# Kernel tuning notes

Hardware: AMD Instinct MI355X
Metric: run time of the kernel (lower is better)

The kernel has to match this reference:

```python
import jax, jax.numpy as jnp
import numpy as np

B, S, D = 2, 1024, 1024
E = 8          # routed experts
I = 1024       # per-expert intermediate
IS = 1024      # shared expert intermediate
TOP_K = 2
NUM_SHARED = 1


def setup_inputs() -> dict:
    key = jax.random.key(0)
    ks = jax.random.split(key, 8)
    scale = 0.02
    return {
        "x": jax.random.normal(ks[0], (B, S, D), dtype=jnp.float32),
        "w_gate": jax.random.normal(ks[1], (D, E), dtype=jnp.float32) * scale,
        "wg": jax.random.normal(ks[2], (E, D, I), dtype=jnp.float32) * scale,  # expert gate_proj
        "wu": jax.random.normal(ks[3], (E, D, I), dtype=jnp.float32) * scale,  # expert up_proj
        "wd": jax.random.normal(ks[4], (E, I, D), dtype=jnp.float32) * scale,  # expert down_proj
        "ws_g": jax.random.normal(ks[5], (NUM_SHARED, D, IS), dtype=jnp.float32) * scale,
        "ws_u": jax.random.normal(ks[6], (NUM_SHARED, D, IS), dtype=jnp.float32) * scale,
        "ws_d": jax.random.normal(ks[7], (NUM_SHARED, IS, D), dtype=jnp.float32) * scale,
    }


def _swiglu(t, w_gate_proj, w_up, w_down):
    # t: [N, D]
    g = t @ w_gate_proj            # [N, I]
    u = t @ w_up                   # [N, I]
    return (jax.nn.silu(g) * u) @ w_down  # [N, D]


def reference(x, w_gate, wg, wu, wd, ws_g, ws_u, ws_d):
    Bb, Ss, Dd = x.shape
    x_flat = x.reshape(Bb * Ss, Dd)                  # [N, D]
    N = x_flat.shape[0]

    # --- router ---
    logits = x_flat @ w_gate                          # [N, E]
    topk_logits, topk_idx = jax.lax.top_k(logits, TOP_K)
    topk_w = jax.nn.softmax(topk_logits, axis=-1)     # [N, K]

    # --- aux load-balancing loss ---
    one_hot = jax.nn.one_hot(topk_idx, E, dtype=jnp.float32)  # [N, K, E]
    f = one_hot.sum(axis=1).mean(axis=0)                       # [E]
    P = jax.nn.softmax(logits, axis=-1).mean(axis=0)           # [E]
    aux_loss = E * jnp.sum(f * P)

    # --- combine weights: cw[n, e] = sum_k topk_w[n,k] * 1[topk_idx[n,k]==e] ---
    cw = jnp.einsum("nk,nke->ne", topk_w, one_hot)             # [N, E]

    # --- routed experts: dense compute over all experts, weighted combine ---
    g = jnp.einsum("nd,edi->eni", x_flat, wg)                  # [E, N, I]
    u = jnp.einsum("nd,edi->eni", x_flat, wu)                  # [E, N, I]
    a = jax.nn.silu(g) * u                                     # [E, N, I]
    y = jnp.einsum("eni,eid->end", a, wd)                      # [E, N, D]
    routed = jnp.einsum("ne,end->nd", cw, y)                   # [N, D]

    # --- shared experts ---
    shared = jnp.zeros_like(x_flat)
    for s in range(NUM_SHARED):
        shared = shared + _swiglu(x_flat, ws_g[s], ws_u[s], ws_d[s])

    out = (routed + shared).reshape(Bb, Ss, Dd)
    return out, aux_loss
```

## Files before the change

### kernel.cpp

```cpp
#include <hip/hip_runtime.h>
#include <math.h>

typedef unsigned short u16;
typedef __attribute__((ext_vector_type(8))) short short8;
typedef __attribute__((ext_vector_type(4))) float f32x4;
typedef __attribute__((ext_vector_type(4))) unsigned short u16x4;
typedef __attribute__((ext_vector_type(8))) unsigned short u16x8;

#define N_TOK 2048
#define DIM 1024
#define OUT_ELEMS 2097152

#define GLDS16(gp, lp) __builtin_amdgcn_global_load_lds( \
    (const __attribute__((address_space(1))) unsigned int*)(gp), \
    (__attribute__((address_space(3))) unsigned int*)(lp), 16, 0, 0)

__device__ __forceinline__ u16 f2bf(float f) {
    union { float f; unsigned u; } v; v.f = f;
    unsigned r = (v.u + 0x7FFFu + ((v.u >> 16) & 1u)) >> 16;
    return (u16)r;
}
__device__ __forceinline__ float bf2f(u16 h) {
    union { unsigned u; float f; } v; v.u = ((unsigned)h) << 16;
    return v.f;
}

__global__ void k_cvt_x(const float* __restrict__ x, u16* __restrict__ xb,
                        int* __restrict__ tlist, int* __restrict__ curs,
                        float* __restrict__ Psum, int* __restrict__ cnt8) {
    int i = blockIdx.x * 256 + threadIdx.x;
    f32x4 v = ((const f32x4*)x)[i];
    u16x4 o;
    o.x = f2bf(v.x); o.y = f2bf(v.y); o.z = f2bf(v.z); o.w = f2bf(v.w);
    ((u16x4*)xb)[i] = o;
    if (i < 2048) tlist[4096 + i] = i;
    if (i < 16) curs[i] = 0;
    if (i < 8) { Psum[i] = 0.f; cnt8[i] = 0; }
}

__global__ void k_cvt_w(const float* __restrict__ wg, const float* __restrict__ wu,
                        const float* __restrict__ wd, const float* __restrict__ wsg,
                        const float* __restrict__ wsu, const float* __restrict__ wsd,
                        u16* __restrict__ wgt, u16* __restrict__ wut,
                        u16* __restrict__ wdt, u16* __restrict__ wsgt,
                        u16* __restrict__ wsut, u16* __restrict__ wsdt) {
    __shared__ float tile[64 * 65];
    int bx = blockIdx.x;
    int mat = bx >> 8;
    int tl  = bx & 255;
    int tr = tl >> 4, tc = tl & 15;
    const float* src; u16* dst;
    if      (mat <  8) { src = wg  + (size_t)mat * 1048576;        dst = wgt + (size_t)mat * 1048576; }
    else if (mat < 16) { src = wu  + (size_t)(mat - 8) * 1048576;  dst = wut + (size_t)(mat - 8) * 1048576; }
    else if (mat < 24) { src = wd  + (size_t)(mat - 16) * 1048576; dst = wdt + (size_t)(mat - 16) * 1048576; }
    else if (mat == 24){ src = wsg; dst = wsgt; }
    else if (mat == 25){ src = wsu; dst = wsut; }
    else               { src = wsd; dst = wsdt; }
    int t = threadIdx.x;
    int col = (t & 15) * 4;
    int r0  = t >> 4;
#pragma unroll
    for (int j = 0; j < 4; j++) {
        int row = r0 + j * 16;
        f32x4 v = *(const f32x4*)(src + (size_t)(tr * 64 + row) * 1024 + tc * 64 + col);
        float* tp = tile + row * 65 + col;
        tp[0] = v.x; tp[1] = v.y; tp[2] = v.z; tp[3] = v.w;
    }
    __syncthreads();
    int kc = (t & 7) * 8;
#pragma unroll
    for (int it = 0; it < 2; it++) {
        int orow = (t >> 3) + it * 32;
        u16x8 o;
#pragma unroll
        for (int i = 0; i < 8; i++) o[i] = f2bf(tile[(kc + i) * 65 + orow]);
        *(u16x8*)(dst + (size_t)(tc * 64 + orow) * 1024 + tr * 64 + kc) = o;
    }
}

__global__ void k_router(const float* __restrict__ x, const float* __restrict__ wgate,
                         int* __restrict__ tidx, float* __restrict__ tw,
                         float* __restrict__ Psum, int* __restrict__ cnt8) {
    __shared__ float sP[8];
    __shared__ int   sC[8];
    int t = threadIdx.x;
    if (t < 8) { sP[t] = 0.f; sC[t] = 0; }
    __syncthreads();
    int wave = t >> 6;
    int lane = t & 63;
    int n = blockIdx.x * 4 + wave;
    const float* xr = x + (size_t)n * DIM;
    float acc[8] = {0.f,0.f,0.f,0.f,0.f,0.f,0.f,0.f};
    for (int d = lane; d < DIM; d += 64) {
        float xv = xr[d];
        const float* wr = wgate + d * 8;
#pragma unroll
        for (int e = 0; e < 8; e++) acc[e] += xv * wr[e];
    }
#pragma unroll
    for (int off = 32; off; off >>= 1) {
#pragma unroll
        for (int e = 0; e < 8; e++) acc[e] += __shfl_xor(acc[e], off);
    }
    if (lane == 0) {
        float mx = acc[0];
#pragma unroll
        for (int e = 1; e < 8; e++) mx = fmaxf(mx, acc[e]);
        float p[8], s = 0.f;
#pragma unroll
        for (int e = 0; e < 8; e++) { p[e] = expf(acc[e] - mx); s += p[e]; }
        float inv = 1.f / s;
#pragma unroll
        for (int e = 0; e < 8; e++) atomicAdd(&sP[e], p[e] * inv);
        int i0 = 0; float b0 = acc[0];
#pragma unroll
        for (int e = 1; e < 8; e++) if (acc[e] > b0) { b0 = acc[e]; i0 = e; }
        int i1 = -1; float b1 = -3.4e38f;
#pragma unroll
        for (int e = 0; e < 8; e++) if (e != i0 && acc[e] > b1) { b1 = acc[e]; i1 = e; }
        float w0 = 1.f / (1.f + expf(b1 - b0));
        tidx[n * 2] = i0; tidx[n * 2 + 1] = i1;
        tw[n * 2] = w0;   tw[n * 2 + 1] = 1.f - w0;
        atomicAdd(&sC[i0], 1);
        atomicAdd(&sC[i1], 1);
    }
    __syncthreads();
    if (t < 8) {
        atomicAdd(&Psum[t], sP[t]);
        atomicAdd(&cnt8[t], sC[t]);
    }
}

__global__ void k_scatter(const int* __restrict__ tidx, const float* __restrict__ Psum,
                          const int* __restrict__ cnt8, int* __restrict__ curs,
                          int* __restrict__ tlist, int* __restrict__ slots,
                          float* __restrict__ out, int* __restrict__ counts,
                          int* __restrict__ offs) {
    __shared__ int s_off[8];
    int t = threadIdx.x;
    if (t == 0) {
        int o = 0;
        for (int e = 0; e < 8; e++) { s_off[e] = o; o += cnt8[e]; }
    }
    __syncthreads();
    if (blockIdx.x == 0 && t == 0) {
        float aux = 0.f;
        for (int e = 0; e < 8; e++) {
            int c = cnt8[e];
            aux += (float)c * Psum[e];
            offs[e] = s_off[e]; counts[e] = c;
        }
        out[OUT_ELEMS] = 8.f * aux / ((float)N_TOK * (float)N_TOK);
        offs[8] = 4096; counts[8] = 2048;
    }
    int n = blockIdx.x * 256 + t;
    if (n < N_TOK) {
#pragma unroll
        for (int k = 0; k < 2; k++) {
            int e = tidx[n * 2 + k];
            int p = atomicAdd(&curs[e], 1);
            int sl = s_off[e] + p;
            tlist[sl] = n;
            slots[n * 2 + k] = sl;
        }
    }
}

__global__ __launch_bounds__(256, 2)
void k_gemm1(const u16* __restrict__ xb, const u16* __restrict__ wgt,
             const u16* __restrict__ wut, const u16* __restrict__ wsgt,
             const u16* __restrict__ wsut, const int* __restrict__ tlist,
             const int* __restrict__ counts, const int* __restrict__ offs,
             u16* __restrict__ H) {
    int bx = blockIdx.x;
    int job = bx >> 7;
    int mt = (bx >> 3) & 15;
    int nt = bx & 7;
    int jcnt = counts[job];
    int m0 = mt << 7;
    if (m0 >= jcnt) return;
    int joff = offs[job];
    int n0 = nt << 7;
    const u16* Bg = (job < 8) ? (wgt + (size_t)job * 1048576) : wsgt;
    const u16* Bu = (job < 8) ? (wut + (size_t)job * 1048576) : wsut;

    __shared__ __attribute__((aligned(128))) u16 As[4096];
    __shared__ __attribute__((aligned(128))) u16 Bgs[4096];
    __shared__ __attribute__((aligned(128))) u16 Bus[4096];

    int t = threadIdx.x;
    int wave = t >> 6, lane = t & 63;
    int ch = (lane & 3) * 8;
    int r0 = (wave * 2 + 0) * 16 + (lane >> 2);
    int r1 = (wave * 2 + 1) * 16 + (lane >> 2);
    int tok0 = tlist[joff + m0 + r0];
    int tok1 = tlist[joff + m0 + r1];
    const u16* a0 = xb + (size_t)tok0 * 1024 + ch;
    const u16* a1 = xb + (size_t)tok1 * 1024 + ch;
    const u16* g0 = Bg + (size_t)(n0 + r0) * 1024 + ch;
    const u16* g1 = Bg + (size_t)(n0 + r1) * 1024 + ch;
    const u16* u0 = Bu + (size_t)(n0 + r0) * 1024 + ch;
    const u16* u1 = Bu + (size_t)(n0 + r1) * 1024 + ch;
    u16* lA0 = As  + (wave * 2 + 0) * 512;  u16* lA1 = As  + (wave * 2 + 1) * 512;
    u16* lG0 = Bgs + (wave * 2 + 0) * 512;  u16* lG1 = Bgs + (wave * 2 + 1) * 512;
    u16* lU0 = Bus + (wave * 2 + 0) * 512;  u16* lU1 = Bus + (wave * 2 + 1) * 512;

    int wm = (wave >> 1) << 6, wn = (wave & 1) << 6;
    int quad = lane >> 4, lr = lane & 15;

    f32x4 accg[4][4], accu[4][4];
    f32x4 zz = {0.f, 0.f, 0.f, 0.f};
#pragma unroll
    for (int i = 0; i < 4; i++)
#pragma unroll
        for (int j = 0; j < 4; j++) { accg[i][j] = zz; accu[i][j] = zz; }

    for (int k0 = 0; k0 < 1024; k0 += 32) {
        GLDS16(a0 + k0, lA0);  GLDS16(a1 + k0, lA1);
        GLDS16(g0 + k0, lG0);  GLDS16(g1 + k0, lG1);
        GLDS16(u0 + k0, lU0);  GLDS16(u1 + k0, lU1);
        __syncthreads();
        short8 af[4], bgf[4], buf[4];
#pragma unroll
        for (int i = 0; i < 4; i++) {
            af[i]  = *(const short8*)(As  + (wm + i * 16 + lr) * 32 + quad * 8);
            bgf[i] = *(const short8*)(Bgs + (wn + i * 16 + lr) * 32 + quad * 8);
            buf[i] = *(const short8*)(Bus + (wn + i * 16 + lr) * 32 + quad * 8);
        }
#pragma unroll
        for (int mi = 0; mi < 4; mi++)
#pragma unroll
            for (int ni = 0; ni < 4; ni++) {
                accg[mi][ni] = __builtin_amdgcn_mfma_f32_16x16x32_bf16(af[mi], bgf[ni], accg[mi][ni], 0, 0, 0);
                accu[mi][ni] = __builtin_amdgcn_mfma_f32_16x16x32_bf16(af[mi], buf[ni], accu[mi][ni], 0, 0, 0);
            }
        __syncthreads();
    }
#pragma unroll
    for (int mi = 0; mi < 4; mi++) {
        int rowb = m0 + wm + mi * 16 + quad * 4;
#pragma unroll
        for (int rr = 0; rr < 4; rr++) {
            int row = rowb + rr;
            if (row < jcnt) {
                size_t base = (size_t)(joff + row) * 1024 + n0 + wn;
#pragma unroll
                for (int ni = 0; ni < 4; ni++) {
                    float g = accg[mi][ni][rr];
                    float u = accu[mi][ni][rr];
                    float h = (g / (1.f + expf(-g))) * u;
                    H[base + ni * 16 + lr] = f2bf(h);
                }
            }
        }
    }
}

__global__ __launch_bounds__(256, 2)
void k_gemm2(const u16* __restrict__ H, const u16* __restrict__ wdt,
             const u16* __restrict__ wsdt, const int* __restrict__ counts,
             const int* __restrict__ offs, u16* __restrict__ Y) {
    int bx = blockIdx.x;
    int job = bx >> 7;
    int mt = (bx >> 3) & 15;
    int nt = bx & 7;
    int jcnt = counts[job];
    int m0 = mt << 7;
    if (m0 >= jcnt) return;
    int joff = offs[job];
    int n0 = nt << 7;
    const u16* Bt = (job < 8) ? (wdt + (size_t)job * 1048576) : wsdt;

    __shared__ __attribute__((aligned(128))) u16 As[4096];
    __shared__ __attribute__((aligned(128))) u16 Bs[4096];

    int t = threadIdx.x;
    int wave = t >> 6, lane = t & 63;
    int ch = (lane & 3) * 8;
    int r0 = (wave * 2 + 0) * 16 + (lane >> 2);
    int r1 = (wave * 2 + 1) * 16 + (lane >> 2);
    const u16* a0 = H + (size_t)(joff + m0 + r0) * 1024 + ch;
    const u16* a1 = H + (size_t)(joff + m0 + r1) * 1024 + ch;
    const u16* b0 = Bt + (size_t)(n0 + r0) * 1024 + ch;
    const u16* b1 = Bt + (size_t)(n0 + r1) * 1024 + ch;
    u16* lA0 = As + (wave * 2 + 0) * 512;  u16* lA1 = As + (wave * 2 + 1) * 512;
    u16* lB0 = Bs + (wave * 2 + 0) * 512;  u16* lB1 = Bs + (wave * 2 + 1) * 512;

    int wm = (wave >> 1) << 6, wn = (wave & 1) << 6;
    int quad = lane >> 4, lr = lane & 15;

    f32x4 acc[4][4];
    f32x4 zz = {0.f, 0.f, 0.f, 0.f};
#pragma unroll
    for (int i = 0; i < 4; i++)
#pragma unroll
        for (int j = 0; j < 4; j++) acc[i][j] = zz;

    for (int k0 = 0; k0 < 1024; k0 += 32) {
        GLDS16(a0 + k0, lA0);  GLDS16(a1 + k0, lA1);
        GLDS16(b0 + k0, lB0);  GLDS16(b1 + k0, lB1);
        __syncthreads();
        short8 af[4], bf[4];
#pragma unroll
        for (int i = 0; i < 4; i++) {
            af[i] = *(const short8*)(As + (wm + i * 16 + lr) * 32 + quad * 8);
            bf[i] = *(const short8*)(Bs + (wn + i * 16 + lr) * 32 + quad * 8);
        }
#pragma unroll
        for (int mi = 0; mi < 4; mi++)
#pragma unroll
            for (int ni = 0; ni < 4; ni++)
                acc[mi][ni] = __builtin_amdgcn_mfma_f32_16x16x32_bf16(af[mi], bf[ni], acc[mi][ni], 0, 0, 0);
        __syncthreads();
    }
#pragma unroll
    for (int mi = 0; mi < 4; mi++) {
        int rowb = m0 + wm + mi * 16 + quad * 4;
#pragma unroll
        for (int rr = 0; rr < 4; rr++) {
            int row = rowb + rr;
            if (row < jcnt) {
                u16* yrow = Y + (size_t)(joff + row) * 1024 + n0 + wn;
#pragma unroll
                for (int ni = 0; ni < 4; ni++)
                    yrow[ni * 16 + lr] = f2bf(acc[mi][ni][rr]);
            }
        }
    }
}

__global__ void k_combine(const u16* __restrict__ Y, const int* __restrict__ slots,
                          const float* __restrict__ tw, float* __restrict__ out) {
    int n = blockIdx.x;
    int d = threadIdx.x;
    int s0 = slots[n * 2], s1 = slots[n * 2 + 1];
    float w0 = tw[n * 2], w1 = tw[n * 2 + 1];
    u16x4 y0 = ((const u16x4*)(Y + (size_t)s0 * 1024))[d];
    u16x4 y1 = ((const u16x4*)(Y + (size_t)s1 * 1024))[d];
    u16x4 ys = ((const u16x4*)(Y + (size_t)(4096 + n) * 1024))[d];
    f32x4 r;
    r.x = w0 * bf2f(y0.x) + w1 * bf2f(y1.x) + bf2f(ys.x);
    r.y = w0 * bf2f(y0.y) + w1 * bf2f(y1.y) + bf2f(ys.y);
    r.z = w0 * bf2f(y0.z) + w1 * bf2f(y1.z) + bf2f(ys.z);
    r.w = w0 * bf2f(y0.w) + w1 * bf2f(y1.w) + bf2f(ys.w);
    ((f32x4*)(out + (size_t)n * 1024))[d] = r;
}

extern "C" void kernel_launch(void* const* d_in, const int* in_sizes, int n_in,
                              void* d_out, int out_size, void* d_ws, size_t ws_size,
                              hipStream_t stream) {
    const float* x     = (const float*)d_in[0];
    const float* wgate = (const float*)d_in[1];
    const float* wg    = (const float*)d_in[2];
    const float* wu    = (const float*)d_in[3];
    const float* wd    = (const float*)d_in[4];
    const float* wsg   = (const float*)d_in[5];
    const float* wsu   = (const float*)d_in[6];
    const float* wsd   = (const float*)d_in[7];
    float* out = (float*)d_out;

    char* ws = (char*)d_ws;
    u16*   xb    = (u16*)(ws + 0);
    u16*   wgt   = (u16*)(ws + 4194304);
    u16*   wut   = (u16*)(ws + 20971520);
    u16*   wdt   = (u16*)(ws + 37748736);
    u16*   wsgt  = (u16*)(ws + 54525952);
    u16*   wsut  = (u16*)(ws + 56623104);
    u16*   wsdt  = (u16*)(ws + 58720256);
    u16*   H     = (u16*)(ws + 60817408);
    u16*   Y     = (u16*)(ws + 4194304);
    int*   tidx  = (int*)(ws + 73400320);
    float* tw    = (float*)(ws + 73416704);
    int*   tlist = (int*)(ws + 73433088);
    int*   slots = (int*)(ws + 73457664);
    int*   counts= (int*)(ws + 73474048);
    int*   offs  = (int*)(ws + 73474112);
    int*   curs  = (int*)(ws + 73474176);
    float* Psum  = (float*)(ws + 73474240);
    int*   cnt8  = (int*)(ws + 73474304);

    k_cvt_x<<<2048, 256, 0, stream>>>(x, xb, tlist, curs, Psum, cnt8);
    k_router<<<512, 256, 0, stream>>>(x, wgate, tidx, tw, Psum, cnt8);
    k_scatter<<<8, 256, 0, stream>>>(tidx, Psum, cnt8, curs, tlist, slots,
                                     out, counts, offs);
    k_cvt_w<<<6912, 256, 0, stream>>>(wg, wu, wd, wsg, wsu, wsd,
                                      wgt, wut, wdt, wsgt, wsut, wsdt);
    k_gemm1<<<1152, 256, 0, stream>>>(xb, wgt, wut, wsgt, wsut, tlist, counts, offs, H);
    k_gemm2<<<1152, 256, 0, stream>>>(H, wdt, wsdt, counts, offs, Y);
    k_combine<<<2048, 256, 0, stream>>>(Y, slots, tw, out);
}
```

Measured before the change: 280.2 us.

## Fuse x bf16 conversion into router and enlarge weight transpose tiles

Removes the standalone x conversion kernel by writing bf16 x inside the router, which already reads x, leaving a tiny init kernel. Rewrites the weight transpose-convert kernel to use 128x128 tiles, converting to bf16 before storing in shared memory and issuing 16 independent loads per thread. This targets the bandwidth-bound weight conversion and launch overhead, at the cost of more registers and shared memory per block and possible LDS bank conflicts on 16-bit column reads.

```diff
diff --git a/kernel.cpp b/kernel.cpp
--- a/kernel.cpp
+++ b/kernel.cpp
@@ -25,15 +25,10 @@
     return v.f;
 }
 
-__global__ void k_cvt_x(const float* __restrict__ x, u16* __restrict__ xb,
-                        int* __restrict__ tlist, int* __restrict__ curs,
-                        float* __restrict__ Psum, int* __restrict__ cnt8) {
+__global__ void k_init(int* __restrict__ tlist, int* __restrict__ curs,
+                       float* __restrict__ Psum, int* __restrict__ cnt8) {
     int i = blockIdx.x * 256 + threadIdx.x;
-    f32x4 v = ((const f32x4*)x)[i];
-    u16x4 o;
-    o.x = f2bf(v.x); o.y = f2bf(v.y); o.z = f2bf(v.z); o.w = f2bf(v.w);
-    ((u16x4*)xb)[i] = o;
-    if (i < 2048) tlist[4096 + i] = i;
+    tlist[4096 + i] = i;
     if (i < 16) curs[i] = 0;
     if (i < 8) { Psum[i] = 0.f; cnt8[i] = 0; }
 }
@@ -44,11 +39,11 @@
                         u16* __restrict__ wgt, u16* __restrict__ wut,
                         u16* __restrict__ wdt, u16* __restrict__ wsgt,
                         u16* __restrict__ wsut, u16* __restrict__ wsdt) {
-    __shared__ float tile[64 * 65];
+    __shared__ u16 tile[128 * 136];
     int bx = blockIdx.x;
-    int mat = bx >> 8;
-    int tl  = bx & 255;
-    int tr = tl >> 4, tc = tl & 15;
+    int mat = bx >> 6;
+    int tl  = bx & 63;
+    int tr = tl >> 3, tc = tl & 7;
     const float* src; u16* dst;
     if      (mat <  8) { src = wg  + (size_t)mat * 1048576;        dst = wgt + (size_t)mat * 1048576; }
     else if (mat < 16) { src = wu  + (size_t)(mat - 8) * 1048576;  dst = wut + (size_t)(mat - 8) * 1048576; }
@@ -57,30 +52,39 @@
     else if (mat == 25){ src = wsu; dst = wsut; }
     else               { src = wsd; dst = wsdt; }
     int t = threadIdx.x;
-    int col = (t & 15) * 4;
-    int r0  = t >> 4;
-#pragma unroll
-    for (int j = 0; j < 4; j++) {
-        int row = r0 + j * 16;
-        f32x4 v = *(const f32x4*)(src + (size_t)(tr * 64 + row) * 1024 + tc * 64 + col);
-        float* tp = tile + row * 65 + col;
-        tp[0] = v.x; tp[1] = v.y; tp[2] = v.z; tp[3] = v.w;
+    int col = (t & 31) * 4;
+    int rb  = t >> 5;
+    const float* sp = src + (size_t)(tr * 128) * 1024 + tc * 128 + col;
+
+    f32x4 v[16];
+#pragma unroll
+    for (int j = 0; j < 16; j++)
+        v[j] = *(const f32x4*)(sp + (size_t)(j * 8 + rb) * 1024);
+#pragma unroll
+    for (int j = 0; j < 16; j++) {
+        int row = j * 8 + rb;
+        u16x4 o;
+        o.x = f2bf(v[j].x); o.y = f2bf(v[j].y); o.z = f2bf(v[j].z); o.w = f2bf(v[j].w);
+        *(u16x4*)(tile + row * 136 + col) = o;
     }
     __syncthreads();
-    int kc = (t & 7) * 8;
-#pragma unroll
-    for (int it = 0; it < 2; it++) {
-        int orow = (t >> 3) + it * 32;
+    int n  = t & 127;
+    int kb = (t >> 7) * 64;
+    u16* drow = dst + (size_t)(tc * 128 + n) * 1024 + tr * 128;
+#pragma unroll
+    for (int j = 0; j < 8; j++) {
+        int kc = kb + j * 8;
         u16x8 o;
 #pragma unroll
-        for (int i = 0; i < 8; i++) o[i] = f2bf(tile[(kc + i) * 65 + orow]);
-        *(u16x8*)(dst + (size_t)(tc * 64 + orow) * 1024 + tr * 64 + kc) = o;
+        for (int i = 0; i < 8; i++) o[i] = tile[(kc + i) * 136 + n];
+        *(u16x8*)(drow + kc) = o;
     }
 }
 
 __global__ void k_router(const float* __restrict__ x, const float* __restrict__ wgate,
-                         int* __restrict__ tidx, float* __restrict__ tw,
-                         float* __restrict__ Psum, int* __restrict__ cnt8) {
+                         u16* __restrict__ xb, int* __restrict__ tidx,
+                         float* __restrict__ tw, float* __restrict__ Psum,
+                         int* __restrict__ cnt8) {
     __shared__ float sP[8];
     __shared__ int   sC[8];
     int t = threadIdx.x;
@@ -90,9 +94,13 @@
     int lane = t & 63;
     int n = blockIdx.x * 4 + wave;
     const float* xr = x + (size_t)n * DIM;
+    u16* xbr = xb + (size_t)n * DIM;
     float acc[8] = {0.f,0.f,0.f,0.f,0.f,0.f,0.f,0.f};
-    for (int d = lane; d < DIM; d += 64) {
+#pragma unroll
+    for (int i = 0; i < 16; i++) {
+        int d = lane + i * 64;
         float xv = xr[d];
+        xbr[d] = f2bf(xv);
         const float* wr = wgate + d * 8;
 #pragma unroll
         for (int e = 0; e < 8; e++) acc[e] += xv * wr[e];
@@ -379,11 +387,11 @@
     float* Psum  = (float*)(ws + 73474240);
     int*   cnt8  = (int*)(ws + 73474304);
 
-    k_cvt_x<<<2048, 256, 0, stream>>>(x, xb, tlist, curs, Psum, cnt8);
-    k_router<<<512, 256, 0, stream>>>(x, wgate, tidx, tw, Psum, cnt8);
+    k_init<<<8, 256, 0, stream>>>(tlist, curs, Psum, cnt8);
+    k_router<<<512, 256, 0, stream>>>(x, wgate, xb, tidx, tw, Psum, cnt8);
     k_scatter<<<8, 256, 0, stream>>>(tidx, Psum, cnt8, curs, tlist, slots,
                                      out, counts, offs);
-    k_cvt_w<<<6912, 256, 0, stream>>>(wg, wu, wd, wsg, wsu, wsd,
+    k_cvt_w<<<1728, 256, 0, stream>>>(wg, wu, wd, wsg, wsu, wsd,
                                       wgt, wut, wdt, wsgt, wsut, wsdt);
     k_gemm1<<<1152, 256, 0, stream>>>(xb, wgt, wut, wsgt, wsut, tlist, counts, offs, H);
     k_gemm2<<<1152, 256, 0, stream>>>(H, wdt, wsdt, counts, offs, Y);
```

Result: no change. 279.6 us (-0.2%).
